# Optimization experiments

Hardware: AMD Instinct MI355X
Metric: run time of the kernel (lower is better)

Reference implementation:

```python
import jax, jax.numpy as jnp
import numpy as np

B, S, D = 8, 1024, 768
H, DQK, DV = 12, 64, 64
DHEAD = 2 * DQK + DV  # 192, interleaved per-head qkv layout
DOUT = 768


def setup_inputs() -> dict:
    key = jax.random.key(0)
    k1, k2, k3, k4 = jax.random.split(key, 4)
    x = jax.random.normal(k1, (B, S, D), dtype=jnp.float32)
    w_qkv = jax.random.normal(k2, (D, H * DHEAD), dtype=jnp.float32) * (D ** -0.5)
    w_out = jax.random.normal(k3, (H * DV, DOUT), dtype=jnp.float32) * ((H * DV) ** -0.5)
    b_out = jax.random.normal(k4, (DOUT,), dtype=jnp.float32) * 0.02
    return {"x": x, "w_qkv": w_qkv, "w_out": w_out, "b_out": b_out}


def reference(x, w_qkv, w_out, b_out):
    scale = DQK ** -0.5
    # Interleaved per-head layout: [B,S,H,DHEAD] then split into q|k|v blocks.
    qkv = (x @ w_qkv).reshape(B, S, H, DHEAD)
    q = qkv[..., :DQK]                 # [B,S,H,DQK]
    k = qkv[..., DQK:2 * DQK]          # [B,S,H,DQK]
    v = qkv[..., 2 * DQK:]             # [B,S,H,DV]
    scores = jnp.einsum("bshd,bthd->bhst", q, k) * scale  # [B,H,S,S]
    attn = jax.nn.softmax(scores, axis=-1)
    out = jnp.einsum("bhst,bthd->bshd", attn, v)           # [B,S,H,DV]
    out = out.reshape(B, S, H * DV)
    return out @ w_out + b_out
```

## Files before the change

### kernel.cpp

```cpp
#include <hip/hip_runtime.h>
#include <hip/hip_bf16.h>
#include <cstdint>

namespace {

constexpr int kB = 8;
constexpr int kS = 1024;
constexpr int kD = 768;
constexpr int kH = 12;
constexpr int kDH = 192;
constexpr int kNQ = kH * kDH;
constexpr int kNK = kH * 128;
constexpr int kM = kB * kS;
constexpr int kDO = 768;

using f32x4 = __attribute__((ext_vector_type(4))) float;
using f32x16 = __attribute__((ext_vector_type(16))) float;
using s16x8 = __attribute__((ext_vector_type(8))) short;
using u16x8 = __attribute__((ext_vector_type(8))) unsigned short;
using u16x4 = __attribute__((ext_vector_type(4))) unsigned short;

__device__ __forceinline__ unsigned short f2bf(float f) {
  union { float f; uint32_t u; } v; v.f = f;
  uint32_t u = v.u;
  u += 0x7FFFu + ((u >> 16) & 1u);
  return (unsigned short)(u >> 16);
}

__device__ __forceinline__ unsigned packbf(float a, float b) {
  float2 f; f.x = a; f.y = b;
  __hip_bfloat162 h = __float22bfloat162_rn(f);
  union { __hip_bfloat162 h; unsigned u; } c; c.h = h;
  return c.u;
}

__device__ __forceinline__ void load_lds16(const void* g, void* l) {
  __builtin_amdgcn_global_load_lds((__attribute__((address_space(1))) void*)g,
                                   (__attribute__((address_space(3))) void*)l,
                                   16, 0, 0);
}

__device__ __forceinline__ s16x8 repack8(int hi, float p0, float p1, float p2, float p3,
                                         float p4, float p5, float p6, float p7) {
  unsigned x0 = packbf(p0, p1);
  unsigned x1 = packbf(p2, p3);
  unsigned x2 = packbf(p4, p5);
  unsigned x3 = packbf(p6, p7);
  unsigned y0 = (unsigned)__shfl_xor((int)x0, 32, 64);
  unsigned y1 = (unsigned)__shfl_xor((int)x1, 32, 64);
  unsigned y2 = (unsigned)__shfl_xor((int)x2, 32, 64);
  unsigned y3 = (unsigned)__shfl_xor((int)x3, 32, 64);
  union { unsigned u[4]; s16x8 v; } r;
  r.u[0] = hi ? y2 : x0;
  r.u[1] = hi ? y3 : x1;
  r.u[2] = hi ? x2 : y0;
  r.u[3] = hi ? x3 : y1;
  return r.v;
}

__device__ __forceinline__ void transpose_tile(const float* __restrict__ w,
                                               unsigned short* __restrict__ wt,
                                               int K, int N, int k0, int n0,
                                               float (*tile)[33]) {
  int tx = threadIdx.x & 31, ty = threadIdx.x >> 5;
  #pragma unroll
  for (int r = 0; r < 32; r += 8)
    tile[ty + r][tx] = w[(size_t)(k0 + ty + r) * N + n0 + tx];
  __syncthreads();
  #pragma unroll
  for (int r = 0; r < 32; r += 8)
    wt[(size_t)(n0 + ty + r) * K + k0 + tx] = f2bf(tile[tx][ty + r]);
}

__global__ __launch_bounds__(256) void prep_kernel(const float* __restrict__ x,
                                                   const float* __restrict__ w_qkv,
                                                   const float* __restrict__ w_out,
                                                   unsigned short* __restrict__ Xb,
                                                   unsigned short* __restrict__ WqT,
                                                   unsigned short* __restrict__ WoT) {
  __shared__ float tile[32][33];
  int id = blockIdx.x;
  if (id < 3072) {
    int i = (id * 256 + threadIdx.x) * 8;
    float4 a = *(const float4*)(x + i);
    float4 b = *(const float4*)(x + i + 4);
    u16x8 o;
    o[0] = f2bf(a.x); o[1] = f2bf(a.y); o[2] = f2bf(a.z); o[3] = f2bf(a.w);
    o[4] = f2bf(b.x); o[5] = f2bf(b.y); o[6] = f2bf(b.z); o[7] = f2bf(b.w);
    *(u16x8*)(Xb + i) = o;
  } else if (id < 4800) {
    int t = id - 3072;
    transpose_tile(w_qkv, WqT, kD, kNQ, (t % 24) * 32, (t / 24) * 32, tile);
  } else {
    int t = id - 4800;
    transpose_tile(w_out, WoT, kDO, kDO, (t % 24) * 32, (t / 24) * 32, tile);
  }
}

template <int MODE>
__global__ __launch_bounds__(256, 2) void gemm_bt_kernel(
    const unsigned short* __restrict__ A,
    const unsigned short* __restrict__ Bt,
    void* __restrict__ Cout,
    unsigned short* __restrict__ Vtg,
    const float* __restrict__ bias,
    int M, int N, int K) {
  __shared__ alignas(16) unsigned short Al[128 * 64];
  __shared__ alignas(16) unsigned short Bl[128 * 64];
  const int nT = N >> 7;
  const int nwg = gridDim.x;
  const int bid = blockIdx.x;
  const int swz = (bid & 7) * (nwg >> 3) + (bid >> 3);
  const int tm = swz / nT, tn = swz % nT;
  const int tid = threadIdx.x;
  const int w = tid >> 6, l = tid & 63;
  const int wr = w >> 1, wc = w & 1;
  const int la = l & 15, g = l >> 4;
  const int sr = l >> 3, sc = l & 7;

  f32x4 acc[4][4] = {};
  const unsigned short* Ag = A + (size_t)(tm * 128) * K;
  const unsigned short* Bg = Bt + (size_t)(tn * 128) * K;

  for (int k0 = 0; k0 < K; k0 += 64) {
    #pragma unroll
    for (int j = 0; j < 4; ++j) {
      int row = w * 32 + j * 8 + sr;
      load_lds16(Ag + (size_t)row * K + k0 + sc * 8, &Al[row * 64 + sc * 8]);
      load_lds16(Bg + (size_t)row * K + k0 + sc * 8, &Bl[row * 64 + sc * 8]);
    }
    __syncthreads();
    #pragma unroll
    for (int kk = 0; kk < 2; ++kk) {
      s16x8 af[4], bfv[4];
      #pragma unroll
      for (int i = 0; i < 4; ++i)
        af[i] = *(const s16x8*)&Al[(wr * 64 + i * 16 + la) * 64 + kk * 32 + g * 8];
      #pragma unroll
      for (int j = 0; j < 4; ++j)
        bfv[j] = *(const s16x8*)&Bl[(wc * 64 + j * 16 + la) * 64 + kk * 32 + g * 8];
      #pragma unroll
      for (int i = 0; i < 4; ++i)
        #pragma unroll
        for (int j = 0; j < 4; ++j)
          acc[i][j] = __builtin_amdgcn_mfma_f32_16x16x32_bf16(bfv[j], af[i], acc[i][j], 0, 0, 0);
    }
    __syncthreads();
  }

  #pragma unroll
  for (int i = 0; i < 4; ++i) {
    int m = tm * 128 + wr * 64 + i * 16 + la;
    #pragma unroll
    for (int j = 0; j < 4; ++j) {
      int n0 = tn * 128 + wc * 64 + j * 16 + g * 4;
      if (MODE == 0) {
        int h = n0 / kDH, colm = n0 % kDH;
        if (colm < 128) {
          unsigned short* C = (unsigned short*)Cout;
          float sc2 = (colm < 64) ? 0.125f : 1.0f;
          u16x4 pv;
          #pragma unroll
          for (int r = 0; r < 4; ++r) pv[r] = f2bf(acc[i][j][r] * sc2);
          *(u16x4*)&C[(size_t)m * kNK + h * 128 + colm] = pv;
        } else {
          int d0 = colm - 128;
          int bb = m >> 10, t = m & 1023;
          #pragma unroll
          for (int r = 0; r < 4; ++r)
            Vtg[((size_t)(bb * kH + h) * 64 + d0 + r) * kS + t] = f2bf(acc[i][j][r]);
        }
      } else {
        float* C = (float*)Cout;
        float4 bv = *(const float4*)&bias[n0];
        float4 o;
        o.x = acc[i][j][0] + bv.x; o.y = acc[i][j][1] + bv.y;
        o.z = acc[i][j][2] + bv.z; o.w = acc[i][j][3] + bv.w;
        *(float4*)&C[(size_t)m * N + n0] = o;
      }
    }
  }
}

__global__ __launch_bounds__(256, 3) void attn_kernel(
    const unsigned short* __restrict__ qk,
    const unsigned short* __restrict__ Vtg,
    unsigned short* __restrict__ Ab) {
  const int id = blockIdx.x;
  const int b = id & 7;
  const int h = (id >> 3) % kH;
  const int qb = id / (kH * 8);
  const int tid = threadIdx.x;
  const int w = tid >> 6, l = tid & 63;
  const int q0 = l & 31, hi = l >> 5;

  __shared__ alignas(16) unsigned short Kl[2][64 * 64];
  __shared__ alignas(16) unsigned short Vl[2][64 * 64];

  const size_t base_bs = (size_t)b * kS;
  const size_t qrow0 = base_bs + (size_t)qb * 128;
  const size_t myq = qrow0 + w * 32 + q0;

  s16x8 qf[4];
  {
    const unsigned short* qp = qk + myq * kNK + h * 128 + hi * 8;
    #pragma unroll
    for (int kg = 0; kg < 4; ++kg) qf[kg] = *(const s16x8*)(qp + kg * 16);
  }

  const int c0 = w * 64 + l;
  const int c1 = 256 + w * 64 + l;
  const int r0 = c0 >> 3, cc0 = (c0 & 7) ^ (r0 & 7);
  const int r1 = c1 >> 3, cc1 = (c1 & 7) ^ (r1 & 7);
  const unsigned short* Kg = qk + base_bs * kNK + h * 128 + 64;
  const unsigned short* Vg = Vtg + (size_t)(b * kH + h) * 64 * kS;

  auto STAGE = [&](int buf, int kt) {
    load_lds16(Kg + (size_t)(kt * 64 + r0) * kNK + cc0 * 8, &Kl[buf][c0 * 8]);
    load_lds16(Kg + (size_t)(kt * 64 + r1) * kNK + cc1 * 8, &Kl[buf][c1 * 8]);
    load_lds16(Vg + (size_t)r0 * kS + kt * 64 + cc0 * 8, &Vl[buf][c0 * 8]);
    load_lds16(Vg + (size_t)r1 * kS + kt * 64 + cc1 * 8, &Vl[buf][c1 * 8]);
  };

  const float LOG2E = 1.44269504088896340736f;
  float m2 = -1e30f;
  float lrow = 0.f;
  f32x16 oacc[2] = {};

  STAGE(0, 0);
  asm volatile("s_waitcnt vmcnt(0)" ::: "memory");
  __builtin_amdgcn_s_barrier();
  __builtin_amdgcn_sched_barrier(0);

  int cur = 0;
  for (int kt = 0; kt < 16; ++kt) {
    if (kt < 15) STAGE(cur ^ 1, kt + 1);

    const unsigned short* Kc = &Kl[cur][0];
    const unsigned short* Vc = &Vl[cur][0];

    f32x16 sacc[2] = {};
    #pragma unroll
    for (int tb = 0; tb < 2; ++tb) {
      const int tl = tb * 32 + q0, xr = tl & 7;
      #pragma unroll
      for (int kg = 0; kg < 4; ++kg) {
        s16x8 kf = *(const s16x8*)&Kc[tl * 64 + (((kg * 2 + hi) ^ xr) * 8)];
        sacc[tb] = __builtin_amdgcn_mfma_f32_32x32x16_bf16(kf, qf[kg], sacc[tb], 0, 0, 0);
      }
    }

    float mx[16];
    #pragma unroll
    for (int r = 0; r < 16; ++r) mx[r] = fmaxf(sacc[0][r], sacc[1][r]);
    #pragma unroll
    for (int s2 = 8; s2 >= 1; s2 >>= 1)
      #pragma unroll
      for (int r = 0; r < s2; ++r) mx[r] = fmaxf(mx[r], mx[r + s2]);
    float pmax = fmaxf(mx[0], __shfl_xor(mx[0], 32, 64));
    float rx2 = pmax * LOG2E;
    if (!__all(rx2 - m2 <= 11.5416f)) {
      float m2n = fmaxf(m2, rx2);
      float corr = exp2f(m2 - m2n);
      m2 = m2n;
      lrow *= corr;
      #pragma unroll
      for (int db = 0; db < 2; ++db)
        #pragma unroll
        for (int r = 0; r < 16; ++r) oacc[db][r] *= corr;
    }

    float p[32];
    #pragma unroll
    for (int tb = 0; tb < 2; ++tb)
      #pragma unroll
      for (int r = 0; r < 16; ++r)
        p[tb * 16 + r] = exp2f(fmaf(sacc[tb][r], LOG2E, -m2));

    float sm[16];
    #pragma unroll
    for (int r = 0; r < 16; ++r) sm[r] = p[r] + p[16 + r];
    #pragma unroll
    for (int s2 = 8; s2 >= 1; s2 >>= 1)
      #pragma unroll
      for (int r = 0; r < s2; ++r) sm[r] += sm[r + s2];
    lrow += sm[0] + __shfl_xor(sm[0], 32, 64);

    s16x8 pb0 = repack8(hi, p[0], p[1], p[2], p[3], p[4], p[5], p[6], p[7]);
    s16x8 pb1 = repack8(hi, p[8], p[9], p[10], p[11], p[12], p[13], p[14], p[15]);
    s16x8 pb2 = repack8(hi, p[16], p[17], p[18], p[19], p[20], p[21], p[22], p[23]);
    s16x8 pb3 = repack8(hi, p[24], p[25], p[26], p[27], p[28], p[29], p[30], p[31]);

    #pragma unroll
    for (int db = 0; db < 2; ++db) {
      const int dl = db * 32 + q0, xr = dl & 7;
      s16x8 v0 = *(const s16x8*)&Vc[dl * 64 + (((0 + hi) ^ xr) * 8)];
      s16x8 v1 = *(const s16x8*)&Vc[dl * 64 + (((2 + hi) ^ xr) * 8)];
      s16x8 v2 = *(const s16x8*)&Vc[dl * 64 + (((4 + hi) ^ xr) * 8)];
      s16x8 v3 = *(const s16x8*)&Vc[dl * 64 + (((6 + hi) ^ xr) * 8)];
      oacc[db] = __builtin_amdgcn_mfma_f32_32x32x16_bf16(v0, pb0, oacc[db], 0, 0, 0);
      oacc[db] = __builtin_amdgcn_mfma_f32_32x32x16_bf16(v1, pb1, oacc[db], 0, 0, 0);
      oacc[db] = __builtin_amdgcn_mfma_f32_32x32x16_bf16(v2, pb2, oacc[db], 0, 0, 0);
      oacc[db] = __builtin_amdgcn_mfma_f32_32x32x16_bf16(v3, pb3, oacc[db], 0, 0, 0);
    }

    __builtin_amdgcn_sched_barrier(0);
    asm volatile("s_waitcnt vmcnt(0)" ::: "memory");
    __builtin_amdgcn_s_barrier();
    __builtin_amdgcn_sched_barrier(0);
    cur ^= 1;
  }

  float inv = 1.0f / lrow;
  unsigned short* dst = Ab + myq * (size_t)(kH * 64) + h * 64;
  #pragma unroll
  for (int db = 0; db < 2; ++db)
    #pragma unroll
    for (int rq = 0; rq < 4; ++rq) {
      union { unsigned u[2]; u16x4 v; } pk;
      pk.u[0] = packbf(oacc[db][rq * 4 + 0] * inv, oacc[db][rq * 4 + 1] * inv);
      pk.u[1] = packbf(oacc[db][rq * 4 + 2] * inv, oacc[db][rq * 4 + 3] * inv);
      *(u16x4*)&dst[db * 32 + rq * 8 + hi * 4] = pk.v;
    }
}

}

extern "C" void kernel_launch(void* const* d_in, const int* in_sizes, int n_in,
                              void* d_out, int out_size, void* d_ws, size_t ws_size,
                              hipStream_t stream) {
  (void)in_sizes; (void)n_in; (void)out_size; (void)ws_size;
  const float* x = (const float*)d_in[0];
  const float* w_qkv = (const float*)d_in[1];
  const float* w_out = (const float*)d_in[2];
  const float* b_out = (const float*)d_in[3];

  unsigned short* Xb = (unsigned short*)d_ws;
  unsigned short* WqT = Xb + (size_t)kM * kD;
  unsigned short* WoT = WqT + (size_t)kNQ * kD;
  unsigned short* QK = WoT + (size_t)kDO * kDO;
  unsigned short* Vtg = QK + (size_t)kM * kNK;
  unsigned short* Ab = Vtg + (size_t)kB * kH * 64 * kS;

  prep_kernel<<<dim3(5376), dim3(256), 0, stream>>>(x, w_qkv, w_out, Xb, WqT, WoT);

  gemm_bt_kernel<0><<<dim3((kM / 128) * (kNQ / 128)), dim3(256), 0, stream>>>(
      Xb, WqT, (void*)QK, Vtg, nullptr, kM, kNQ, kD);

  attn_kernel<<<dim3((kS / 128) * kH * kB), dim3(256), 0, stream>>>(QK, Vtg, Ab);

  gemm_bt_kernel<1><<<dim3((kM / 128) * (kDO / 128)), dim3(256), 0, stream>>>(
      Ab, WoT, d_out, nullptr, b_out, kM, kDO, kH * 64);
}
```

Baseline: 209.8 us.

## Split attention KV range across two wave groups and merge partial softmax results

The attention block grows from 256 to 512 threads. Two groups of four waves each process half of the key/value tiles for the same query rows, then merge their partial outputs, running max and running sum through shared memory at the end. This halves the serial loop length per wave and raises the number of waves available to hide latency. s_setprio is also raised around the MFMA sections. In exchange, LDS use grows to 64KB per block, there is a final merge step with an extra barrier, and occupancy may be limited by registers and LDS.

```diff
diff --git a/kernel.cpp b/kernel.cpp
--- a/kernel.cpp
+++ b/kernel.cpp
@@ -182,7 +182,7 @@
   }
 }
 
-__global__ __launch_bounds__(256, 3) void attn_kernel(
+__global__ __launch_bounds__(512, 4) void attn_kernel(
     const unsigned short* __restrict__ qk,
     const unsigned short* __restrict__ Vtg,
     unsigned short* __restrict__ Ab) {
@@ -192,14 +192,16 @@
   const int qb = id / (kH * 8);
   const int tid = threadIdx.x;
   const int w = tid >> 6, l = tid & 63;
+  const int wg = w & 3, half = w >> 2;
   const int q0 = l & 31, hi = l >> 5;
 
-  __shared__ alignas(16) unsigned short Kl[2][64 * 64];
-  __shared__ alignas(16) unsigned short Vl[2][64 * 64];
+  __shared__ alignas(16) unsigned char smem[65536];
+  unsigned short* Kbase = (unsigned short*)smem;
+  unsigned short* Vbase = (unsigned short*)(smem + 32768);
 
   const size_t base_bs = (size_t)b * kS;
   const size_t qrow0 = base_bs + (size_t)qb * 128;
-  const size_t myq = qrow0 + w * 32 + q0;
+  const size_t myq = qrow0 + wg * 32 + q0;
 
   s16x8 qf[4];
   {
@@ -208,18 +210,20 @@
     for (int kg = 0; kg < 4; ++kg) qf[kg] = *(const s16x8*)(qp + kg * 16);
   }
 
-  const int c0 = w * 64 + l;
-  const int c1 = 256 + w * 64 + l;
+  const int c0 = wg * 64 + l;
+  const int c1 = 256 + wg * 64 + l;
   const int r0 = c0 >> 3, cc0 = (c0 & 7) ^ (r0 & 7);
   const int r1 = c1 >> 3, cc1 = (c1 & 7) ^ (r1 & 7);
   const unsigned short* Kg = qk + base_bs * kNK + h * 128 + 64;
   const unsigned short* Vg = Vtg + (size_t)(b * kH + h) * 64 * kS;
 
-  auto STAGE = [&](int buf, int kt) {
-    load_lds16(Kg + (size_t)(kt * 64 + r0) * kNK + cc0 * 8, &Kl[buf][c0 * 8]);
-    load_lds16(Kg + (size_t)(kt * 64 + r1) * kNK + cc1 * 8, &Kl[buf][c1 * 8]);
-    load_lds16(Vg + (size_t)r0 * kS + kt * 64 + cc0 * 8, &Vl[buf][c0 * 8]);
-    load_lds16(Vg + (size_t)r1 * kS + kt * 64 + cc1 * 8, &Vl[buf][c1 * 8]);
+  auto STAGE = [&](int buf, int ktg) {
+    unsigned short* Kd = Kbase + (half * 2 + buf) * 4096;
+    unsigned short* Vd = Vbase + (half * 2 + buf) * 4096;
+    load_lds16(Kg + (size_t)(ktg * 64 + r0) * kNK + cc0 * 8, Kd + c0 * 8);
+    load_lds16(Kg + (size_t)(ktg * 64 + r1) * kNK + cc1 * 8, Kd + c1 * 8);
+    load_lds16(Vg + (size_t)r0 * kS + ktg * 64 + cc0 * 8, Vd + c0 * 8);
+    load_lds16(Vg + (size_t)r1 * kS + ktg * 64 + cc1 * 8, Vd + c1 * 8);
   };
 
   const float LOG2E = 1.44269504088896340736f;
@@ -227,19 +231,20 @@
   float lrow = 0.f;
   f32x16 oacc[2] = {};
 
-  STAGE(0, 0);
+  STAGE(0, half * 8);
   asm volatile("s_waitcnt vmcnt(0)" ::: "memory");
   __builtin_amdgcn_s_barrier();
   __builtin_amdgcn_sched_barrier(0);
 
   int cur = 0;
-  for (int kt = 0; kt < 16; ++kt) {
-    if (kt < 15) STAGE(cur ^ 1, kt + 1);
-
-    const unsigned short* Kc = &Kl[cur][0];
-    const unsigned short* Vc = &Vl[cur][0];
+  for (int kt = 0; kt < 8; ++kt) {
+    if (kt < 7) STAGE(cur ^ 1, half * 8 + kt + 1);
+
+    const unsigned short* Kc = Kbase + (half * 2 + cur) * 4096;
+    const unsigned short* Vc = Vbase + (half * 2 + cur) * 4096;
 
     f32x16 sacc[2] = {};
+    __builtin_amdgcn_s_setprio(1);
     #pragma unroll
     for (int tb = 0; tb < 2; ++tb) {
       const int tl = tb * 32 + q0, xr = tl & 7;
@@ -249,6 +254,7 @@
         sacc[tb] = __builtin_amdgcn_mfma_f32_32x32x16_bf16(kf, qf[kg], sacc[tb], 0, 0, 0);
       }
     }
+    __builtin_amdgcn_s_setprio(0);
 
     float mx[16];
     #pragma unroll
@@ -291,6 +297,7 @@
     s16x8 pb2 = repack8(hi, p[16], p[17], p[18], p[19], p[20], p[21], p[22], p[23]);
     s16x8 pb3 = repack8(hi, p[24], p[25], p[26], p[27], p[28], p[29], p[30], p[31]);
 
+    __builtin_amdgcn_s_setprio(1);
     #pragma unroll
     for (int db = 0; db < 2; ++db) {
       const int dl = db * 32 + q0, xr = dl & 7;
@@ -303,6 +310,7 @@
       oacc[db] = __builtin_amdgcn_mfma_f32_32x32x16_bf16(v2, pb2, oacc[db], 0, 0, 0);
       oacc[db] = __builtin_amdgcn_mfma_f32_32x32x16_bf16(v3, pb3, oacc[db], 0, 0, 0);
     }
+    __builtin_amdgcn_s_setprio(0);
 
     __builtin_amdgcn_sched_barrier(0);
     asm volatile("s_waitcnt vmcnt(0)" ::: "memory");
@@ -311,17 +319,39 @@
     cur ^= 1;
   }
 
-  float inv = 1.0f / lrow;
-  unsigned short* dst = Ab + myq * (size_t)(kH * 64) + h * 64;
-  #pragma unroll
-  for (int db = 0; db < 2; ++db)
-    #pragma unroll
-    for (int rq = 0; rq < 4; ++rq) {
-      union { unsigned u[2]; u16x4 v; } pk;
-      pk.u[0] = packbf(oacc[db][rq * 4 + 0] * inv, oacc[db][rq * 4 + 1] * inv);
-      pk.u[1] = packbf(oacc[db][rq * 4 + 2] * inv, oacc[db][rq * 4 + 3] * inv);
-      *(u16x4*)&dst[db * 32 + rq * 8 + hi * 4] = pk.v;
-    }
+  float* cbuf = (float*)smem;
+  if (half == 1) {
+    float* dstb = cbuf + ((wg * 64 + l) * 34);
+    #pragma unroll
+    for (int db = 0; db < 2; ++db)
+      #pragma unroll
+      for (int r = 0; r < 16; ++r) dstb[db * 16 + r] = oacc[db][r];
+    dstb[32] = m2;
+    dstb[33] = lrow;
+  }
+  __syncthreads();
+  if (half == 0) {
+    const float* srcb = cbuf + ((wg * 64 + l) * 34);
+    float m2p = srcb[32], lp = srcb[33];
+    float mm = fmaxf(m2, m2p);
+    float ca = exp2f(m2 - mm), cb2 = exp2f(m2p - mm);
+    float inv = 1.0f / (lrow * ca + lp * cb2);
+    float sa = ca * inv, sb = cb2 * inv;
+    unsigned short* dst = Ab + myq * (size_t)(kH * 64) + h * 64;
+    #pragma unroll
+    for (int db = 0; db < 2; ++db)
+      #pragma unroll
+      for (int rq = 0; rq < 4; ++rq) {
+        float v0 = oacc[db][rq * 4 + 0] * sa + srcb[db * 16 + rq * 4 + 0] * sb;
+        float v1 = oacc[db][rq * 4 + 1] * sa + srcb[db * 16 + rq * 4 + 1] * sb;
+        float v2 = oacc[db][rq * 4 + 2] * sa + srcb[db * 16 + rq * 4 + 2] * sb;
+        float v3 = oacc[db][rq * 4 + 3] * sa + srcb[db * 16 + rq * 4 + 3] * sb;
+        union { unsigned u[2]; u16x4 v; } pk;
+        pk.u[0] = packbf(v0, v1);
+        pk.u[1] = packbf(v2, v3);
+        *(u16x4*)&dst[db * 32 + rq * 8 + hi * 4] = pk.v;
+      }
+  }
 }
 
 }
@@ -347,7 +377,7 @@
   gemm_bt_kernel<0><<<dim3((kM / 128) * (kNQ / 128)), dim3(256), 0, stream>>>(
       Xb, WqT, (void*)QK, Vtg, nullptr, kM, kNQ, kD);
 
-  attn_kernel<<<dim3((kS / 128) * kH * kB), dim3(256), 0, stream>>>(QK, Vtg, Ab);
+  attn_kernel<<<dim3((kS / 128) * kH * kB), dim3(512), 0, stream>>>(QK, Vtg, Ab);
 
   gemm_bt_kernel<1><<<dim3((kM / 128) * (kDO / 128)), dim3(256), 0, stream>>>(
       Ab, WoT, d_out, nullptr, b_out, kM, kDO, kH * 64);
```

Result: no change. 208.3 us (-0.7%).
